# Optimization experiments

Hardware: AMD Instinct MI355X
Metric: run time of the kernel (lower is better)

## Reference

```python
import jax, jax.numpy as jnp
import numpy as np

B, H, N, D = 4, 8, 2048, 64  # d_model=512, n_heads=8 -> d_head=64
MASK_PROB = 0.1
SCALE = D ** -0.5


def setup_inputs() -> dict:
    key = jax.random.key(0)
    kq, kk, kv, km = jax.random.split(key, 4)
    q = jax.random.normal(kq, (B, H, N, D), dtype=jnp.float32)
    k = jax.random.normal(kk, (B, H, N, D), dtype=jnp.float32)
    v = jax.random.normal(kv, (B, H, N, D), dtype=jnp.float32)
    # torch.bernoulli(full(..., prob)): 1 with prob=mask_prob -> dropped
    mask = jax.random.bernoulli(km, MASK_PROB, (B, H, N, N))
    return {"q": q, "k": k, "v": v, "mask": mask}


def reference(q, k, v, mask):
    # [B,H,N,N] scores: QK^T * scale -> tanh -> zero where mask is True
    scores = jnp.tanh(jnp.einsum("bhnd,bhmd->bhnm", q, k) * SCALE)
    scores = scores * (~mask).astype(scores.dtype)
    return jnp.einsum("bhnm,bhmd->bhnd", scores, v)
```

## Files before the change

kernel.cpp:

```cpp
#include <hip/hip_runtime.h>

namespace {

constexpr int N = 2048;
constexpr int D = 64;
constexpr float SCALE = 0.125f;
constexpr int LK = 72;
constexpr int LV = 68;
constexpr int NT = N / 64;

typedef __attribute__((ext_vector_type(8))) short bf16x8;
typedef __attribute__((ext_vector_type(4))) short short4v;
typedef __attribute__((ext_vector_type(2))) short short2v;
typedef __attribute__((ext_vector_type(4))) float f32x4;
typedef __attribute__((ext_vector_type(4))) int   int4v;

__device__ inline short f2bf(float x) {
  union { float f; unsigned u; } a; a.f = x;
  unsigned r = a.u + 0x7fffu + ((a.u >> 16) & 1u);
  return (short)(r >> 16);
}

#if __has_builtin(__builtin_amdgcn_cvt_pk_bf16_f32)
typedef __attribute__((ext_vector_type(2))) __bf16 bfv2;
__device__ inline short2v pk_bf(float lo, float hi) {
  bfv2 t = __builtin_amdgcn_cvt_pk_bf16_f32(lo, hi);
  return __builtin_bit_cast(short2v, t);
}
#else
__device__ inline short2v pk_bf(float lo, float hi) {
  short2v r; r[0] = f2bf(lo); r[1] = f2bf(hi); return r;
}
#endif

__device__ inline short4v pk4(float4 f) {
  short2v a = pk_bf(f.x, f.y), b = pk_bf(f.z, f.w);
  short4v r; r[0] = a[0]; r[1] = a[1]; r[2] = b[0]; r[3] = b[1];
  return r;
}

__device__ inline float fast_tanh(float x) {
  float e = __builtin_amdgcn_exp2f(x * 2.885390081777927f);
  return 1.0f - 2.0f * __builtin_amdgcn_rcpf(e + 1.0f);
}

}

__global__ __launch_bounds__(256, 4) void attn_tanh_kernel(
    const float* __restrict__ Q, const float* __restrict__ K,
    const float* __restrict__ V, const int* __restrict__ M,
    float* __restrict__ O)
{
  __shared__ __align__(16) short k_s[64 * LK];
  __shared__ __align__(16) short s_s[64 * LK];
  __shared__ __align__(16) short vt_s[64 * LV];

  const int tid  = threadIdx.x;
  const int wave = tid >> 6;
  const int lane = tid & 63;
  const int l15  = lane & 15;
  const int quad = lane >> 4;

  const int bh = blockIdx.x >> 5;
  const int q0 = (blockIdx.x & 31) * 64;

  const float* qp = Q + (size_t)bh * N * D;
  const float* kp = K + (size_t)bh * N * D;
  const float* vp = V + (size_t)bh * N * D;
  const int*   mp = M + (size_t)bh * N * N;
  float* op = O + (size_t)bh * N * D;

  bf16x8 qf[2];
  {
    const float* qrow = qp + (size_t)(q0 + wave * 16 + l15) * D + quad * 8;
#pragma unroll
    for (int ks = 0; ks < 2; ++ks) {
      float4 f0 = *(const float4*)(qrow + ks * 32);
      float4 f1 = *(const float4*)(qrow + ks * 32 + 4);
      short4v lo = pk4(f0), hi = pk4(f1);
      bf16x8 t;
      t[0]=lo[0]; t[1]=lo[1]; t[2]=lo[2]; t[3]=lo[3];
      t[4]=hi[0]; t[5]=hi[1]; t[6]=hi[2]; t[7]=hi[3];
      qf[ks] = t;
    }
  }

  const int r0 = tid >> 4;
  const int c4 = (tid & 15) << 2;

  float4 kreg[4];
  float  vreg[16];
  int4v  mreg[4];

  const float* vbase = vp + (size_t)(wave * 16) * D + lane;
  const int*   mbase = mp + (size_t)(q0 + wave * 16 + l15) * N + quad * 4;

#pragma unroll
  for (int i = 0; i < 4; ++i)
    kreg[i] = *(const float4*)(kp + (size_t)(i * 16 + r0) * D + c4);
#pragma unroll
  for (int i = 0; i < 16; ++i)
    vreg[i] = vbase[(size_t)i * D];
#pragma unroll
  for (int ct = 0; ct < 4; ++ct)
    mreg[ct] = __builtin_nontemporal_load((const int4v*)(mbase + ct * 16));

  f32x4 o_acc[4];
#pragma unroll
  for (int i = 0; i < 4; ++i) o_acc[i] = (f32x4){0.f, 0.f, 0.f, 0.f};

  for (int kt = 0; kt < NT; ++kt) {
    __syncthreads();

#pragma unroll
    for (int i = 0; i < 4; ++i)
      *(short4v*)(&k_s[(i * 16 + r0) * LK + c4]) = pk4(kreg[i]);
#pragma unroll
    for (int c = 0; c < 4; ++c) {
      short2v p0 = pk_bf(vreg[4 * c + 0], vreg[4 * c + 1]);
      short2v p1 = pk_bf(vreg[4 * c + 2], vreg[4 * c + 3]);
      short4v vv; vv[0] = p0[0]; vv[1] = p0[1]; vv[2] = p1[0]; vv[3] = p1[1];
      *(short4v*)(&vt_s[lane * LV + wave * 16 + 4 * c]) = vv;
    }
    __syncthreads();

#pragma unroll
    for (int ct = 0; ct < 4; ++ct) {
      f32x4 acc = {0.f, 0.f, 0.f, 0.f};
#pragma unroll
      for (int ksi = 0; ksi < 2; ++ksi) {
        bf16x8 a = *(const bf16x8*)(&k_s[(ct * 16 + l15) * LK + ksi * 32 + quad * 8]);
        acc = __builtin_amdgcn_mfma_f32_16x16x32_bf16(a, qf[ksi], acc, 0, 0, 0);
      }
      float s0 = mreg[ct][0] ? 0.f : fast_tanh(acc[0] * SCALE);
      float s1 = mreg[ct][1] ? 0.f : fast_tanh(acc[1] * SCALE);
      float s2 = mreg[ct][2] ? 0.f : fast_tanh(acc[2] * SCALE);
      float s3 = mreg[ct][3] ? 0.f : fast_tanh(acc[3] * SCALE);
      short2v p0 = pk_bf(s0, s1), p1 = pk_bf(s2, s3);
      short4v sv; sv[0] = p0[0]; sv[1] = p0[1]; sv[2] = p1[0]; sv[3] = p1[1];
      *(short4v*)(&s_s[(wave * 16 + l15) * LK + ct * 16 + quad * 4]) = sv;
    }

    if (kt + 1 < NT) {
      const float* kpt = kp + (size_t)(kt + 1) * 64 * D;
#pragma unroll
      for (int i = 0; i < 4; ++i)
        kreg[i] = *(const float4*)(kpt + (size_t)(i * 16 + r0) * D + c4);
      const float* vpt = vbase + (size_t)(kt + 1) * 64 * D;
#pragma unroll
      for (int i = 0; i < 16; ++i)
        vreg[i] = vpt[(size_t)i * D];
      const int* mb = mbase + (size_t)(kt + 1) * 64;
#pragma unroll
      for (int ct = 0; ct < 4; ++ct)
        mreg[ct] = __builtin_nontemporal_load((const int4v*)(mb + ct * 16));
    }

#pragma unroll
    for (int ksi = 0; ksi < 2; ++ksi) {
      bf16x8 a = *(const bf16x8*)(&s_s[(wave * 16 + l15) * LK + ksi * 32 + quad * 8]);
#pragma unroll
      for (int nt = 0; nt < 4; ++nt) {
        const short* vb = &vt_s[(nt * 16 + l15) * LV + ksi * 32 + quad * 8];
        short4v lo = *(const short4v*)(vb);
        short4v hi = *(const short4v*)(vb + 4);
        bf16x8 b = __builtin_shufflevector(lo, hi, 0, 1, 2, 3, 4, 5, 6, 7);
        o_acc[nt] = __builtin_amdgcn_mfma_f32_16x16x32_bf16(a, b, o_acc[nt], 0, 0, 0);
      }
    }
  }

#pragma unroll
  for (int nt = 0; nt < 4; ++nt) {
#pragma unroll
    for (int r = 0; r < 4; ++r) {
      op[(q0 + wave * 16 + quad * 4 + r) * D + nt * 16 + l15] = o_acc[nt][r];
    }
  }
}

extern "C" void kernel_launch(void* const* d_in, const int* in_sizes, int n_in,
                              void* d_out, int out_size, void* d_ws, size_t ws_size,
                              hipStream_t stream) {
  const float* q = (const float*)d_in[0];
  const float* k = (const float*)d_in[1];
  const float* v = (const float*)d_in[2];
  const int* m = (const int*)d_in[3];
  float* out = (float*)d_out;

  attn_tanh_kernel<<<dim3(1024), dim3(256), 0, stream>>>(q, k, v, m, out);
}
```

Baseline: 763.3 us.

## Pre-convert K/V to bf16 in workspace and reorder block-to-head mapping

Adds a pre-pass kernel that converts K and V to bf16 in the workspace, so the attention kernel streams half the K/V bytes and skips per-tile conversion. It also remaps block indices so consecutive blocks cover different heads rather than consecutive query tiles of the same head, which changes L2 sharing of K/V. The work is done every call, and the extra launch and conversion traffic add cost. Loads are refactored into lambdas, with a register copy of the mask for the current tile.

```diff
diff --git a/kernel.cpp b/kernel.cpp
--- a/kernel.cpp
+++ b/kernel.cpp
@@ -8,6 +8,7 @@
 constexpr int LK = 72;
 constexpr int LV = 68;
 constexpr int NT = N / 64;
+constexpr size_t NKV = (size_t)4 * 8 * 2048 * 64;
 
 typedef __attribute__((ext_vector_type(8))) short bf16x8;
 typedef __attribute__((ext_vector_type(4))) short short4v;
@@ -46,9 +47,22 @@
 
 }
 
+__global__ __launch_bounds__(256) void cvt_kv_bf16(
+    const float* __restrict__ K, const float* __restrict__ V,
+    short* __restrict__ KB, short* __restrict__ VB)
+{
+  const int n4 = (int)(NKV / 4);
+  const int stride = gridDim.x * blockDim.x;
+  for (int j = blockIdx.x * blockDim.x + threadIdx.x; j < n4; j += stride) {
+    ((short4v*)KB)[j] = pk4(((const float4*)K)[j]);
+    ((short4v*)VB)[j] = pk4(((const float4*)V)[j]);
+  }
+}
+
+template <bool BF>
 __global__ __launch_bounds__(256, 4) void attn_tanh_kernel(
-    const float* __restrict__ Q, const float* __restrict__ K,
-    const float* __restrict__ V, const int* __restrict__ M,
+    const float* __restrict__ Q, const void* __restrict__ Kp,
+    const void* __restrict__ Vp, const int* __restrict__ M,
     float* __restrict__ O)
 {
   __shared__ __align__(16) short k_s[64 * LK];
@@ -61,12 +75,10 @@
   const int l15  = lane & 15;
   const int quad = lane >> 4;
 
-  const int bh = blockIdx.x >> 5;
-  const int q0 = (blockIdx.x & 31) * 64;
+  const int bh = blockIdx.x & 31;
+  const int q0 = (blockIdx.x >> 5) * 64;
 
   const float* qp = Q + (size_t)bh * N * D;
-  const float* kp = K + (size_t)bh * N * D;
-  const float* vp = V + (size_t)bh * N * D;
   const int*   mp = M + (size_t)bh * N * N;
   float* op = O + (size_t)bh * N * D;
 
@@ -85,25 +97,84 @@
     }
   }
 
+  const int*   mbase = mp + (size_t)(q0 + wave * 16 + l15) * N + quad * 4;
+  int4v mreg[4];
+
   const int r0 = tid >> 4;
   const int c4 = (tid & 15) << 2;
-
   float4 kreg[4];
-  float  vreg[16];
-  int4v  mreg[4];
-
-  const float* vbase = vp + (size_t)(wave * 16) * D + lane;
-  const int*   mbase = mp + (size_t)(q0 + wave * 16 + l15) * N + quad * 4;
-
-#pragma unroll
-  for (int i = 0; i < 4; ++i)
-    kreg[i] = *(const float4*)(kp + (size_t)(i * 16 + r0) * D + c4);
-#pragma unroll
-  for (int i = 0; i < 16; ++i)
-    vreg[i] = vbase[(size_t)i * D];
-#pragma unroll
-  for (int ct = 0; ct < 4; ++ct)
-    mreg[ct] = __builtin_nontemporal_load((const int4v*)(mbase + ct * 16));
+  float  vregf[16];
+  const int krow = tid >> 3;
+  const int kcol = (tid & 7) * 8;
+  bf16x8 kreg2[2];
+  short  vregb[16];
+
+  const float* kpf = nullptr; const float* vpf = nullptr;
+  const short* kpb = nullptr; const short* vpb = nullptr;
+  const float* vbasef = nullptr; const short* vbaseb = nullptr;
+  if constexpr (BF) {
+    kpb = (const short*)Kp + (size_t)bh * N * D;
+    vpb = (const short*)Vp + (size_t)bh * N * D;
+    vbaseb = vpb + (size_t)(wave * 16) * D + lane;
+  } else {
+    kpf = (const float*)Kp + (size_t)bh * N * D;
+    vpf = (const float*)Vp + (size_t)bh * N * D;
+    vbasef = vpf + (size_t)(wave * 16) * D + lane;
+  }
+
+  auto issue_loads = [&](int kt1) {
+    if constexpr (BF) {
+      const short* kt_ = kpb + (size_t)kt1 * 64 * D;
+#pragma unroll
+      for (int i = 0; i < 2; ++i)
+        kreg2[i] = *(const bf16x8*)(kt_ + (size_t)(krow + i * 32) * D + kcol);
+      const short* vt_ = vbaseb + (size_t)kt1 * 64 * D;
+#pragma unroll
+      for (int i = 0; i < 16; ++i)
+        vregb[i] = vt_[(size_t)i * D];
+    } else {
+      const float* kt_ = kpf + (size_t)kt1 * 64 * D;
+#pragma unroll
+      for (int i = 0; i < 4; ++i)
+        kreg[i] = *(const float4*)(kt_ + (size_t)(i * 16 + r0) * D + c4);
+      const float* vt_ = vbasef + (size_t)kt1 * 64 * D;
+#pragma unroll
+      for (int i = 0; i < 16; ++i)
+        vregf[i] = vt_[(size_t)i * D];
+    }
+    const int* mb = mbase + (size_t)kt1 * 64;
+#pragma unroll
+    for (int ct = 0; ct < 4; ++ct)
+      mreg[ct] = __builtin_nontemporal_load((const int4v*)(mb + ct * 16));
+  };
+
+  auto write_kv = [&]() {
+    if constexpr (BF) {
+#pragma unroll
+      for (int i = 0; i < 2; ++i)
+        *(bf16x8*)(&k_s[(krow + i * 32) * LK + kcol]) = kreg2[i];
+#pragma unroll
+      for (int c = 0; c < 4; ++c) {
+        short4v vv;
+        vv[0] = vregb[4*c+0]; vv[1] = vregb[4*c+1];
+        vv[2] = vregb[4*c+2]; vv[3] = vregb[4*c+3];
+        *(short4v*)(&vt_s[lane * LV + wave * 16 + 4 * c]) = vv;
+      }
+    } else {
+#pragma unroll
+      for (int i = 0; i < 4; ++i)
+        *(short4v*)(&k_s[(i * 16 + r0) * LK + c4]) = pk4(kreg[i]);
+#pragma unroll
+      for (int c = 0; c < 4; ++c) {
+        short2v p0 = pk_bf(vregf[4*c+0], vregf[4*c+1]);
+        short2v p1 = pk_bf(vregf[4*c+2], vregf[4*c+3]);
+        short4v vv; vv[0]=p0[0]; vv[1]=p0[1]; vv[2]=p1[0]; vv[3]=p1[1];
+        *(short4v*)(&vt_s[lane * LV + wave * 16 + 4 * c]) = vv;
+      }
+    }
+  };
+
+  issue_loads(0);
 
   f32x4 o_acc[4];
 #pragma unroll
@@ -111,18 +182,12 @@
 
   for (int kt = 0; kt < NT; ++kt) {
     __syncthreads();
-
-#pragma unroll
-    for (int i = 0; i < 4; ++i)
-      *(short4v*)(&k_s[(i * 16 + r0) * LK + c4]) = pk4(kreg[i]);
-#pragma unroll
-    for (int c = 0; c < 4; ++c) {
-      short2v p0 = pk_bf(vreg[4 * c + 0], vreg[4 * c + 1]);
-      short2v p1 = pk_bf(vreg[4 * c + 2], vreg[4 * c + 3]);
-      short4v vv; vv[0] = p0[0]; vv[1] = p0[1]; vv[2] = p1[0]; vv[3] = p1[1];
-      *(short4v*)(&vt_s[lane * LV + wave * 16 + 4 * c]) = vv;
-    }
+    write_kv();
     __syncthreads();
+
+    int4v mcur[4];
+#pragma unroll
+    for (int ct = 0; ct < 4; ++ct) mcur[ct] = mreg[ct];
 
 #pragma unroll
     for (int ct = 0; ct < 4; ++ct) {
@@ -132,29 +197,16 @@
         bf16x8 a = *(const bf16x8*)(&k_s[(ct * 16 + l15) * LK + ksi * 32 + quad * 8]);
         acc = __builtin_amdgcn_mfma_f32_16x16x32_bf16(a, qf[ksi], acc, 0, 0, 0);
       }
-      float s0 = mreg[ct][0] ? 0.f : fast_tanh(acc[0] * SCALE);
-      float s1 = mreg[ct][1] ? 0.f : fast_tanh(acc[1] * SCALE);
-      float s2 = mreg[ct][2] ? 0.f : fast_tanh(acc[2] * SCALE);
-      float s3 = mreg[ct][3] ? 0.f : fast_tanh(acc[3] * SCALE);
+      float s0 = mcur[ct][0] ? 0.f : fast_tanh(acc[0] * SCALE);
+      float s1 = mcur[ct][1] ? 0.f : fast_tanh(acc[1] * SCALE);
+      float s2 = mcur[ct][2] ? 0.f : fast_tanh(acc[2] * SCALE);
+      float s3 = mcur[ct][3] ? 0.f : fast_tanh(acc[3] * SCALE);
       short2v p0 = pk_bf(s0, s1), p1 = pk_bf(s2, s3);
-      short4v sv; sv[0] = p0[0]; sv[1] = p0[1]; sv[2] = p1[0]; sv[3] = p1[1];
+      short4v sv; sv[0]=p0[0]; sv[1]=p0[1]; sv[2]=p1[0]; sv[3]=p1[1];
       *(short4v*)(&s_s[(wave * 16 + l15) * LK + ct * 16 + quad * 4]) = sv;
     }
 
-    if (kt + 1 < NT) {
-      const float* kpt = kp + (size_t)(kt + 1) * 64 * D;
-#pragma unroll
-      for (int i = 0; i < 4; ++i)
-        kreg[i] = *(const float4*)(kpt + (size_t)(i * 16 + r0) * D + c4);
-      const float* vpt = vbase + (size_t)(kt + 1) * 64 * D;
-#pragma unroll
-      for (int i = 0; i < 16; ++i)
-        vreg[i] = vpt[(size_t)i * D];
-      const int* mb = mbase + (size_t)(kt + 1) * 64;
-#pragma unroll
-      for (int ct = 0; ct < 4; ++ct)
-        mreg[ct] = __builtin_nontemporal_load((const int4v*)(mb + ct * 16));
-    }
+    if (kt + 1 < NT) issue_loads(kt + 1);
 
 #pragma unroll
     for (int ksi = 0; ksi < 2; ++ksi) {
@@ -185,8 +237,15 @@
   const float* q = (const float*)d_in[0];
   const float* k = (const float*)d_in[1];
   const float* v = (const float*)d_in[2];
-  const int* m = (const int*)d_in[3];
+  const int*   m = (const int*)d_in[3];
   float* out = (float*)d_out;
 
-  attn_tanh_kernel<<<dim3(1024), dim3(256), 0, stream>>>(q, k, v, m, out);
-}
+  if (ws_size >= NKV * 2 * sizeof(short)) {
+    short* kb = (short*)d_ws;
+    short* vb = kb + NKV;
+    cvt_kv_bf16<<<dim3(2048), dim3(256), 0, stream>>>(k, v, kb, vb);
+    attn_tanh_kernel<true><<<dim3(1024), dim3(256), 0, stream>>>(q, kb, vb, m, out);
+  } else {
+    attn_tanh_kernel<false><<<dim3(1024), dim3(256), 0, stream>>>(q, k, v, m, out);
+  }
+}
```

Result: no change. 776.5 us (+1.7%).
